# Optimization experiments

Hardware: AMD Instinct MI355X
Metric: run time of the kernel (lower is better)

Reference implementation:

```python
import jax
import jax.numpy as jnp
import numpy as np
from jax import lax

T, N, F_IN, H, E = 8, 10000, 128, 64, 160000


def setup_inputs() -> dict:
    key = jax.random.key(0)
    ks = jax.random.split(key, 8)
    s = 0.05
    return {
        "x": jax.random.normal(ks[0], (T, N, F_IN), jnp.float32),
        "edge_index": jax.random.randint(ks[1], (T, 2, E), 0, N, dtype=jnp.int64),
        "W_gcn": jax.random.normal(ks[2], (F_IN, H), jnp.float32) * s,
        "b_gcn": jnp.zeros((H,), jnp.float32),
        "W_ih": jax.random.normal(ks[3], (4 * H, H), jnp.float32) * s,
        "W_hh": jax.random.normal(ks[4], (4 * H, H), jnp.float32) * s,
        "b_ih": jnp.zeros((4 * H,), jnp.float32),
        "b_hh": jnp.zeros((4 * H,), jnp.float32),
    }


def _gcn_one(x, edge_index, W, b):
    # PyG GCNConv: transform then symmetric-normalized propagation with self-loops.
    h = x @ W  # [N, H]
    loop = jnp.arange(N, dtype=edge_index.dtype)
    src = jnp.concatenate([edge_index[0], loop])
    dst = jnp.concatenate([edge_index[1], loop])
    deg = jax.ops.segment_sum(jnp.ones_like(dst, dtype=h.dtype), dst, num_segments=N)
    dinv = lax.rsqrt(deg)  # deg >= 1 thanks to self-loops
    norm = dinv[src] * dinv[dst]  # [E+N]
    out = jax.ops.segment_sum(h[src] * norm[:, None], dst, num_segments=N)
    return out + b


def _lstm(xs, W_ih, W_hh, b_ih, b_hh):
    # batch_first LSTM: batch = T (graphs), sequence = N (nodes)
    xs_t = jnp.swapaxes(xs, 0, 1)  # [N, T, H]
    h0 = jnp.zeros((xs.shape[0], H), xs.dtype)
    c0 = jnp.zeros_like(h0)

    def step(carry, xt):
        h, c = carry
        gates = xt @ W_ih.T + b_ih + h @ W_hh.T + b_hh  # [T, 4H]
        i, f, g, o = jnp.split(gates, 4, axis=-1)  # torch gate order i,f,g,o
        i = jax.nn.sigmoid(i)
        f = jax.nn.sigmoid(f)
        g = jnp.tanh(g)
        o = jax.nn.sigmoid(o)
        c = f * c + i * g
        h = o * jnp.tanh(c)
        return (h, c), h

    _, hs = lax.scan(step, (h0, c0), xs_t)  # hs [N, T, H]
    return jnp.swapaxes(hs, 0, 1)  # [T, N, H]


def reference(x, edge_index, W_gcn, b_gcn, W_ih, W_hh, b_ih, b_hh):
    # per-graph GCNConv -> ReLU (dropout is identity in eval mode)
    gcn_out = jax.vmap(lambda xi, ei: _gcn_one(xi, ei, W_gcn, b_gcn))(x, edge_index)
    gcn_out = jax.nn.relu(gcn_out)  # [T, N, H]; squeeze(0) is a no-op for T>1
    return _lstm(gcn_out, W_ih, W_hh, b_ih, b_hh)
```

## Files before the change

kernel.cpp:

```cpp
#include <hip/hip_runtime.h>

#define Tn 8
#define Nn 10000
#define FIN 128
#define Hh 64
#define En 160000
#define NODES (Tn * Nn)
#define CAP 64

#define CHUNK 20
#define NCHT (Nn / CHUNK)
#define CHAINS (Tn * NCHT)
#define WARM 96
#define STEPS (WARM + CHUNK)

typedef _Float16 h8 __attribute__((ext_vector_type(8)));
typedef _Float16 h4 __attribute__((ext_vector_type(4)));
typedef float f4v __attribute__((ext_vector_type(4)));
typedef unsigned short u16x8 __attribute__((ext_vector_type(8)));

__device__ __forceinline__ float sigm(float x) {
    float e = __builtin_amdgcn_exp2f(-1.4426950408889634f * x);
    return __builtin_amdgcn_rcpf(1.0f + e);
}
__device__ __forceinline__ float tanh_(float x) {
    float e = __builtin_amdgcn_exp2f(2.8853900817779268f * x);
    return 1.0f - 2.0f * __builtin_amdgcn_rcpf(1.0f + e);
}

__device__ __forceinline__ int eget(const void* ei, int is32, size_t pos) {
    return is32 ? ((const int*)ei)[pos] : (int)((const long long*)ei)[pos];
}

__device__ __forceinline__ int detect32(const void* ei, int* s_aux) {
    unsigned aa = 0;
    for (int i = threadIdx.x; i < 4096; i += 256) aa |= ((const unsigned*)ei)[2 * i + 1];
    if (threadIdx.x == 0) *s_aux = 0;
    __syncthreads();
    if (aa) atomicOr(s_aux, 1);
    __syncthreads();
    return *s_aux;
}

__global__ void k_fill(const void* ei, int* cnt, unsigned short* elist) {
    __shared__ int s_aux;
    int is32 = detect32(ei, &s_aux);
    int t = blockIdx.x & 7;
    int e = (blockIdx.x >> 3) * 256 + threadIdx.x;
    int src = eget(ei, is32, (size_t)t * 2 * En + e);
    int dst = eget(ei, is32, (size_t)t * 2 * En + En + e);
    int node = t * Nn + dst;
    int pos = atomicAdd(&cnt[node], 1) & (CAP - 1);
    elist[(size_t)node * CAP + pos] = (unsigned short)src;
}

__global__ void k_gcn(const float* __restrict__ x, const float* __restrict__ Wg,
                      const int* __restrict__ cnt, float* __restrict__ dinv,
                      _Float16* __restrict__ hs) {
    __shared__ __align__(16) float smem[FIN * Hh + 16 * FIN];
    int tid = threadIdx.x;
    float* wl = smem;
    float* xs = smem + FIN * Hh;
    for (int i = tid; i < FIN * Hh / 4; i += 256)
        ((float4*)wl)[i] = ((const float4*)Wg)[i];
    int r0 = blockIdx.x * 16;
    const float4* x4 = (const float4*)(x + (size_t)r0 * FIN);
    ((float4*)xs)[tid] = x4[tid];
    ((float4*)xs)[tid + 256] = x4[tid + 256];
    __syncthreads();
    int cc = tid & 63, jg = tid >> 6;
    float acc[4] = {0.f, 0.f, 0.f, 0.f};
#pragma unroll 4
    for (int k = 0; k < FIN; k++) {
        float wv = wl[k * Hh + cc];
#pragma unroll
        for (int r = 0; r < 4; r++) acc[r] += xs[(jg * 4 + r) * FIN + k] * wv;
    }
#pragma unroll
    for (int r = 0; r < 4; r++) {
        int row = r0 + jg * 4 + r;
        float dv = rsqrtf((float)cnt[row] + 1.0f);
        if (cc == 0) dinv[row] = dv;
        hs[(size_t)row * Hh + cc] = (_Float16)(acc[r] * dv);
    }
}

__global__ void k_g(const int* __restrict__ cnt, const unsigned short* __restrict__ elist,
                    const _Float16* __restrict__ hs, const float* __restrict__ dinv,
                    const float* __restrict__ bg, _Float16* __restrict__ gbuf) {
    int tid = threadIdx.x;
    int jj = tid >> 4;
    int l16 = tid & 15;
    int grp = blockIdx.x * 16 + jj;
    int nedge = cnt[grp];
    const unsigned short* el = elist + (size_t)grp * CAP;
    const _Float16* ht = hs + (size_t)(grp / Nn) * Nn * Hh;
    float4 acc = {0.f, 0.f, 0.f, 0.f};
    for (int k = 0; k < nedge; k += 16) {
        u16x8 sa = *(const u16x8*)(el + k);
        u16x8 sb = *(const u16x8*)(el + k + 8);
        h4 v[16];
#pragma unroll
        for (int i = 0; i < 8; i++) v[i] = ((const h4*)(ht + (size_t)sa[i] * Hh))[l16];
#pragma unroll
        for (int i = 0; i < 8; i++) v[8 + i] = ((const h4*)(ht + (size_t)sb[i] * Hh))[l16];
#pragma unroll
        for (int i = 0; i < 16; i++) {
            float m = (k + i < nedge) ? 1.f : 0.f;
            acc.x += m * (float)v[i][0];
            acc.y += m * (float)v[i][1];
            acc.z += m * (float)v[i][2];
            acc.w += m * (float)v[i][3];
        }
    }
    float dd = dinv[grp];
    h4 hv = ((const h4*)(hs + (size_t)grp * Hh))[l16];
    float4 bgv = ((const float4*)bg)[l16];
    h4 gq;
    gq[0] = (_Float16)fmaxf((acc.x + (float)hv[0]) * dd + bgv.x, 0.f);
    gq[1] = (_Float16)fmaxf((acc.y + (float)hv[1]) * dd + bgv.y, 0.f);
    gq[2] = (_Float16)fmaxf((acc.z + (float)hv[2]) * dd + bgv.z, 0.f);
    gq[3] = (_Float16)fmaxf((acc.w + (float)hv[3]) * dd + bgv.w, 0.f);
    *(h4*)(gbuf + (size_t)grp * Hh + l16 * 4) = gq;
}

__global__ void __launch_bounds__(256, 1) k_lstm(const _Float16* __restrict__ gbuf,
                                                 const float* __restrict__ Wih,
                                                 const float* __restrict__ Whh,
                                                 const float* __restrict__ bih,
                                                 const float* __restrict__ bhh,
                                                 float* __restrict__ out) {
    __shared__ __align__(16) _Float16 hb[2][16][72];
    __shared__ __align__(16) _Float16 gb2[2][16][72];
    int tid = threadIdx.x;
    int w = tid >> 6;
    int lane = tid & 63;
    int l = lane & 15;
    int kg = lane >> 4;
    int col = w * 16 + l;

    h8 bh_[4][2], bg_[4][2];
    float bias[4];
#pragma unroll
    for (int q = 0; q < 4; q++) {
        int row = q * 64 + col;
        bias[q] = bih[row] + bhh[row];
#pragma unroll
        for (int half = 0; half < 2; half++) {
            const float* srch = Whh + (size_t)row * 64 + half * 32 + kg * 8;
            const float* srcg = Wih + (size_t)row * 64 + half * 32 + kg * 8;
            h8 th, tg;
#pragma unroll
            for (int j = 0; j < 8; j++) {
                th[j] = (_Float16)srch[j];
                tg[j] = (_Float16)srcg[j];
            }
            bh_[q][half] = th;
            bg_[q][half] = tg;
        }
    }

    float* ob[4];
    int nv[4], msk[4];
#pragma unroll
    for (int r = 0; r < 4; r++) {
        int g = blockIdx.x * 16 + 4 * kg + r;
        int tt = g / NCHT;
        int ch = g - tt * NCHT;
        nv[r] = ch * CHUNK - WARM;
        msk[r] = (ch == 0);
        ob[r] = out + (size_t)tt * Nn * 64 + col;
    }

    int sm = tid >> 4, sc = tid & 15;
    int gsid = blockIdx.x * 16 + sm;
    int stt = gsid / NCHT, sch = gsid - stt * NCHT;
    int nvs = sch * CHUNK - WARM;
    const _Float16* gp = gbuf + (size_t)stt * Nn * Hh + sc * 4;

    for (int i = tid; i < 2 * 16 * 72; i += 256) ((_Float16*)hb)[i] = (_Float16)0.f;
    {
        int n0 = nvs < 0 ? 0 : nvs;
        *(h4*)&gb2[0][sm][sc * 4] = *(const h4*)(gp + (size_t)n0 * Hh);
    }
    h4 pf[4];
#pragma unroll
    for (int d = 0; d < 4; d++) {
        int n = nvs + 1 + d;
        n = n < 0 ? 0 : (n > Nn - 1 ? Nn - 1 : n);
        pf[d] = *(const h4*)(gp + (size_t)n * Hh);
    }
    __syncthreads();

    float c0 = 0.f, c1 = 0.f, c2 = 0.f, c3 = 0.f;

#define MF(a, b, c) __builtin_amdgcn_mfma_f32_16x16x32_f16(a, b, c, 0, 0, 0)

#define GATES(r, cc, DO_STORE, s)                                \
    {                                                            \
        float iv = sigm(acc0[r]);                                \
        float fv = sigm(acc1[r]);                                \
        float gv = tanh_(acc2[r]);                               \
        float ov = sigm(acc3[r]);                                \
        cc = fv * cc + iv * gv;                                  \
        float hv = ov * tanh_(cc);                               \
        hb[((s) + 1) & 1][4 * kg + r][col] = (_Float16)hv;       \
        if (DO_STORE) ob[r][(size_t)(nv[r] + (s)) * 64] = hv;    \
    }

#define STEP(s, u, DO_STORE)                                                        \
    {                                                                               \
        h8 ah0 = *(const h8*)&hb[(s) & 1][l][kg * 8];                               \
        h8 ah1 = *(const h8*)&hb[(s) & 1][l][32 + kg * 8];                          \
        h8 ag0 = *(const h8*)&gb2[(s) & 1][l][kg * 8];                              \
        h8 ag1 = *(const h8*)&gb2[(s) & 1][l][32 + kg * 8];                         \
        f4v acc0 = {bias[0], bias[0], bias[0], bias[0]};                            \
        f4v acc1 = {bias[1], bias[1], bias[1], bias[1]};                            \
        f4v acc2 = {bias[2], bias[2], bias[2], bias[2]};                            \
        f4v acc3 = {bias[3], bias[3], bias[3], bias[3]};                            \
        acc0 = MF(ag0, bg_[0][0], acc0);                                            \
        acc1 = MF(ag0, bg_[1][0], acc1);                                            \
        acc2 = MF(ag0, bg_[2][0], acc2);                                            \
        acc3 = MF(ag0, bg_[3][0], acc3);                                            \
        acc0 = MF(ag1, bg_[0][1], acc0);                                            \
        acc1 = MF(ag1, bg_[1][1], acc1);                                            \
        acc2 = MF(ag1, bg_[2][1], acc2);                                            \
        acc3 = MF(ag1, bg_[3][1], acc3);                                            \
        acc0 = MF(ah0, bh_[0][0], acc0);                                            \
        acc1 = MF(ah0, bh_[1][0], acc1);                                            \
        acc2 = MF(ah0, bh_[2][0], acc2);                                            \
        acc3 = MF(ah0, bh_[3][0], acc3);                                            \
        acc0 = MF(ah1, bh_[0][1], acc0);                                            \
        acc1 = MF(ah1, bh_[1][1], acc1);                                            \
        acc2 = MF(ah1, bh_[2][1], acc2);                                            \
        acc3 = MF(ah1, bh_[3][1], acc3);                                            \
        *(h4*)&gb2[((s) + 1) & 1][sm][sc * 4] = pf[u];                              \
        {                                                                           \
            int np = nvs + (s) + 5;                                                 \
            np = np < 0 ? 0 : (np > Nn - 1 ? Nn - 1 : np);                          \
            pf[u] = *(const h4*)(gp + (size_t)np * Hh);                             \
        }                                                                           \
        GATES(0, c0, DO_STORE, s)                                                   \
        GATES(1, c1, DO_STORE, s)                                                   \
        GATES(2, c2, DO_STORE, s)                                                   \
        GATES(3, c3, DO_STORE, s)                                                   \
        asm volatile("s_waitcnt lgkmcnt(0)\n\ts_barrier" ::: "memory");             \
    }

    for (int s4 = 0; s4 < WARM; s4 += 4) {
        STEP(s4 + 0, 0, 0)
        STEP(s4 + 1, 1, 0)
        STEP(s4 + 2, 2, 0)
        STEP(s4 + 3, 3, 0)
    }
    if (msk[0]) { c0 = 0.f; hb[WARM & 1][4 * kg + 0][col] = (_Float16)0.f; }
    if (msk[1]) { c1 = 0.f; hb[WARM & 1][4 * kg + 1][col] = (_Float16)0.f; }
    if (msk[2]) { c2 = 0.f; hb[WARM & 1][4 * kg + 2][col] = (_Float16)0.f; }
    if (msk[3]) { c3 = 0.f; hb[WARM & 1][4 * kg + 3][col] = (_Float16)0.f; }
    asm volatile("s_waitcnt lgkmcnt(0)\n\ts_barrier" ::: "memory");
    for (int s4 = WARM; s4 < STEPS; s4 += 4) {
        STEP(s4 + 0, 0, 1)
        STEP(s4 + 1, 1, 1)
        STEP(s4 + 2, 2, 1)
        STEP(s4 + 3, 3, 1)
    }
#undef STEP
#undef GATES
#undef MF
}

extern "C" void kernel_launch(void* const* d_in, const int* in_sizes, int n_in,
                              void* d_out, int out_size, void* d_ws, size_t ws_size,
                              hipStream_t stream) {
    const float* x = (const float*)d_in[0];
    const void* ei = d_in[1];
    const float* Wg = (const float*)d_in[2];
    const float* bg = (const float*)d_in[3];
    const float* Wih = (const float*)d_in[4];
    const float* Whh = (const float*)d_in[5];
    const float* bih = (const float*)d_in[6];
    const float* bhh = (const float*)d_in[7];
    float* out = (float*)d_out;

    char* ws = (char*)d_ws;
    _Float16* gbuf = (_Float16*)(ws);
    _Float16* hs = (_Float16*)(ws + 10240000);
    float* dinv = (float*)(ws + 20480000);
    int* cnt = (int*)(ws + 20800000);
    unsigned short* elist = (unsigned short*)(ws + 21120000);

    hipMemsetAsync(cnt, 0, NODES * sizeof(int), stream);
    k_fill<<<Tn * En / 256, 256, 0, stream>>>(ei, cnt, elist);
    k_gcn<<<NODES / 16, 256, 0, stream>>>(x, Wg, cnt, dinv, hs);
    k_g<<<NODES / 16, 256, 0, stream>>>(cnt, elist, hs, dinv, bg, gbuf);
    k_lstm<<<CHAINS / 16, 256, 0, stream>>>(gbuf, Wih, Whh, bih, bhh, out);
}
```

Baseline: 280.9 us.

## Load LSTM input operands directly to registers and restructure GCN smem layout

The LSTM kernel no longer stages the GCN output through a shared-memory double buffer. Each lane loads its MFMA A-operand fragments straight from global memory into registers, prefetched two steps ahead. The input-projection MFMAs are issued before the h-dependent LDS reads, so they can overlap the previous step's hidden-state writes. The separate mask/barrier block at the warm-up boundary is replaced by an in-loop reset check. Separately, the GCN matmul transposes W into padded shared memory and uses float4 reads with explicit FMAs, which cuts the number of LDS instructions. The trade-off is a shorter prefetch distance, so global-load latency is less hidden in the serial recurrence.

```diff
diff --git a/kernel.cpp b/kernel.cpp
--- a/kernel.cpp
+++ b/kernel.cpp
@@ -57,24 +57,34 @@
 __global__ void k_gcn(const float* __restrict__ x, const float* __restrict__ Wg,
                       const int* __restrict__ cnt, float* __restrict__ dinv,
                       _Float16* __restrict__ hs) {
-    __shared__ __align__(16) float smem[FIN * Hh + 16 * FIN];
+    __shared__ __align__(16) float wl[64][132];
+    __shared__ __align__(16) float xs[16][132];
     int tid = threadIdx.x;
-    float* wl = smem;
-    float* xs = smem + FIN * Hh;
-    for (int i = tid; i < FIN * Hh / 4; i += 256)
-        ((float4*)wl)[i] = ((const float4*)Wg)[i];
+    for (int i = tid; i < FIN * Hh; i += 256) {
+        int k = i >> 6, c = i & 63;
+        wl[c][k] = Wg[i];
+    }
     int r0 = blockIdx.x * 16;
     const float4* x4 = (const float4*)(x + (size_t)r0 * FIN);
-    ((float4*)xs)[tid] = x4[tid];
-    ((float4*)xs)[tid + 256] = x4[tid + 256];
+    {
+        int i0 = tid, i1 = tid + 256;
+        *(float4*)&xs[i0 >> 5][(i0 & 31) * 4] = x4[i0];
+        *(float4*)&xs[i1 >> 5][(i1 & 31) * 4] = x4[i1];
+    }
     __syncthreads();
     int cc = tid & 63, jg = tid >> 6;
     float acc[4] = {0.f, 0.f, 0.f, 0.f};
-#pragma unroll 4
-    for (int k = 0; k < FIN; k++) {
-        float wv = wl[k * Hh + cc];
-#pragma unroll
-        for (int r = 0; r < 4; r++) acc[r] += xs[(jg * 4 + r) * FIN + k] * wv;
+#pragma unroll 8
+    for (int k = 0; k < FIN; k += 4) {
+        float4 wv = *(const float4*)&wl[cc][k];
+#pragma unroll
+        for (int r = 0; r < 4; r++) {
+            float4 xv = *(const float4*)&xs[jg * 4 + r][k];
+            acc[r] = __builtin_fmaf(wv.x, xv.x, acc[r]);
+            acc[r] = __builtin_fmaf(wv.y, xv.y, acc[r]);
+            acc[r] = __builtin_fmaf(wv.z, xv.z, acc[r]);
+            acc[r] = __builtin_fmaf(wv.w, xv.w, acc[r]);
+        }
     }
 #pragma unroll
     for (int r = 0; r < 4; r++) {
@@ -131,7 +141,6 @@
                                                  const float* __restrict__ bhh,
                                                  float* __restrict__ out) {
     __shared__ __align__(16) _Float16 hb[2][16][72];
-    __shared__ __align__(16) _Float16 gb2[2][16][72];
     int tid = threadIdx.x;
     int w = tid >> 6;
     int lane = tid & 63;
@@ -161,108 +170,98 @@
     }
 
     float* ob[4];
-    int nv[4], msk[4];
+    int nv[4], rst[4];
 #pragma unroll
     for (int r = 0; r < 4; r++) {
         int g = blockIdx.x * 16 + 4 * kg + r;
         int tt = g / NCHT;
         int ch = g - tt * NCHT;
         nv[r] = ch * CHUNK - WARM;
-        msk[r] = (ch == 0);
+        rst[r] = -nv[r];
         ob[r] = out + (size_t)tt * Nn * 64 + col;
     }
 
-    int sm = tid >> 4, sc = tid & 15;
-    int gsid = blockIdx.x * 16 + sm;
-    int stt = gsid / NCHT, sch = gsid - stt * NCHT;
-    int nvs = sch * CHUNK - WARM;
-    const _Float16* gp = gbuf + (size_t)stt * Nn * Hh + sc * 4;
+    int gid = blockIdx.x * 16 + l;
+    int gtt = gid / NCHT;
+    int gch = gid - gtt * NCHT;
+    int gnv = gch * CHUNK - WARM;
+    const _Float16* gb = gbuf + (size_t)gtt * Nn * Hh + kg * 8;
 
     for (int i = tid; i < 2 * 16 * 72; i += 256) ((_Float16*)hb)[i] = (_Float16)0.f;
+    __syncthreads();
+
+    h8 agA0, agA1, agB0, agB1;
     {
-        int n0 = nvs < 0 ? 0 : nvs;
-        *(h4*)&gb2[0][sm][sc * 4] = *(const h4*)(gp + (size_t)n0 * Hh);
-    }
-    h4 pf[4];
-#pragma unroll
-    for (int d = 0; d < 4; d++) {
-        int n = nvs + 1 + d;
-        n = n < 0 ? 0 : (n > Nn - 1 ? Nn - 1 : n);
-        pf[d] = *(const h4*)(gp + (size_t)n * Hh);
-    }
-    __syncthreads();
-
+        int n0 = gnv < 0 ? 0 : gnv;
+        agA0 = *(const h8*)(gb + (size_t)n0 * Hh);
+        agA1 = *(const h8*)(gb + (size_t)n0 * Hh + 32);
+        int n1 = gnv + 1;
+        n1 = n1 < 0 ? 0 : n1;
+        agB0 = *(const h8*)(gb + (size_t)n1 * Hh);
+        agB1 = *(const h8*)(gb + (size_t)n1 * Hh + 32);
+    }
     float c0 = 0.f, c1 = 0.f, c2 = 0.f, c3 = 0.f;
 
 #define MF(a, b, c) __builtin_amdgcn_mfma_f32_16x16x32_f16(a, b, c, 0, 0, 0)
 
-#define GATES(r, cc, DO_STORE, s)                                \
+#define GATES(r, cc, DO_STORE, s, P)                             \
     {                                                            \
-        float iv = sigm(acc0[r]);                                \
-        float fv = sigm(acc1[r]);                                \
-        float gv = tanh_(acc2[r]);                               \
-        float ov = sigm(acc3[r]);                                \
+        float iv = sigm(a0[r]);                                  \
+        float fv = sigm(a1[r]);                                  \
+        float gv = tanh_(a2[r]);                                 \
+        float ov = sigm(a3[r]);                                  \
         cc = fv * cc + iv * gv;                                  \
         float hv = ov * tanh_(cc);                               \
-        hb[((s) + 1) & 1][4 * kg + r][col] = (_Float16)hv;       \
+        if ((s) + 1 == rst[r]) { cc = 0.f; hv = 0.f; }           \
+        hb[(P) ^ 1][4 * kg + r][col] = (_Float16)hv;             \
         if (DO_STORE) ob[r][(size_t)(nv[r] + (s)) * 64] = hv;    \
     }
 
-#define STEP(s, u, DO_STORE)                                                        \
+#define STEP(s, P, G0, G1, DO_STORE)                                                \
     {                                                                               \
-        h8 ah0 = *(const h8*)&hb[(s) & 1][l][kg * 8];                               \
-        h8 ah1 = *(const h8*)&hb[(s) & 1][l][32 + kg * 8];                          \
-        h8 ag0 = *(const h8*)&gb2[(s) & 1][l][kg * 8];                              \
-        h8 ag1 = *(const h8*)&gb2[(s) & 1][l][32 + kg * 8];                         \
-        f4v acc0 = {bias[0], bias[0], bias[0], bias[0]};                            \
-        f4v acc1 = {bias[1], bias[1], bias[1], bias[1]};                            \
-        f4v acc2 = {bias[2], bias[2], bias[2], bias[2]};                            \
-        f4v acc3 = {bias[3], bias[3], bias[3], bias[3]};                            \
-        acc0 = MF(ag0, bg_[0][0], acc0);                                            \
-        acc1 = MF(ag0, bg_[1][0], acc1);                                            \
-        acc2 = MF(ag0, bg_[2][0], acc2);                                            \
-        acc3 = MF(ag0, bg_[3][0], acc3);                                            \
-        acc0 = MF(ag1, bg_[0][1], acc0);                                            \
-        acc1 = MF(ag1, bg_[1][1], acc1);                                            \
-        acc2 = MF(ag1, bg_[2][1], acc2);                                            \
-        acc3 = MF(ag1, bg_[3][1], acc3);                                            \
-        acc0 = MF(ah0, bh_[0][0], acc0);                                            \
-        acc1 = MF(ah0, bh_[1][0], acc1);                                            \
-        acc2 = MF(ah0, bh_[2][0], acc2);                                            \
-        acc3 = MF(ah0, bh_[3][0], acc3);                                            \
-        acc0 = MF(ah1, bh_[0][1], acc0);                                            \
-        acc1 = MF(ah1, bh_[1][1], acc1);                                            \
-        acc2 = MF(ah1, bh_[2][1], acc2);                                            \
-        acc3 = MF(ah1, bh_[3][1], acc3);                                            \
-        *(h4*)&gb2[((s) + 1) & 1][sm][sc * 4] = pf[u];                              \
+        f4v a0 = {bias[0], bias[0], bias[0], bias[0]};                              \
+        f4v a1 = {bias[1], bias[1], bias[1], bias[1]};                              \
+        f4v a2 = {bias[2], bias[2], bias[2], bias[2]};                              \
+        f4v a3 = {bias[3], bias[3], bias[3], bias[3]};                              \
+        a0 = MF(G0, bg_[0][0], a0);                                                 \
+        a1 = MF(G0, bg_[1][0], a1);                                                 \
+        a2 = MF(G0, bg_[2][0], a2);                                                 \
+        a3 = MF(G0, bg_[3][0], a3);                                                 \
+        a0 = MF(G1, bg_[0][1], a0);                                                 \
+        a1 = MF(G1, bg_[1][1], a1);                                                 \
+        a2 = MF(G1, bg_[2][1], a2);                                                 \
+        a3 = MF(G1, bg_[3][1], a3);                                                 \
         {                                                                           \
-            int np = nvs + (s) + 5;                                                 \
+            int np = gnv + (s) + 2;                                                 \
             np = np < 0 ? 0 : (np > Nn - 1 ? Nn - 1 : np);                          \
-            pf[u] = *(const h4*)(gp + (size_t)np * Hh);                             \
+            const _Float16* gq = gb + (size_t)np * Hh;                              \
+            G0 = *(const h8*)gq;                                                    \
+            G1 = *(const h8*)(gq + 32);                                             \
         }                                                                           \
-        GATES(0, c0, DO_STORE, s)                                                   \
-        GATES(1, c1, DO_STORE, s)                                                   \
-        GATES(2, c2, DO_STORE, s)                                                   \
-        GATES(3, c3, DO_STORE, s)                                                   \
+        h8 ah0 = *(const h8*)&hb[P][l][kg * 8];                                     \
+        h8 ah1 = *(const h8*)&hb[P][l][32 + kg * 8];                                \
+        a0 = MF(ah0, bh_[0][0], a0);                                                \
+        a1 = MF(ah0, bh_[1][0], a1);                                                \
+        a2 = MF(ah0, bh_[2][0], a2);                                                \
+        a3 = MF(ah0, bh_[3][0], a3);                                                \
+        a0 = MF(ah1, bh_[0][1], a0);                                                \
+        a1 = MF(ah1, bh_[1][1], a1);                                                \
+        a2 = MF(ah1, bh_[2][1], a2);                                                \
+        a3 = MF(ah1, bh_[3][1], a3);                                                \
+        GATES(0, c0, DO_STORE, s, P)                                                \
+        GATES(1, c1, DO_STORE, s, P)                                                \
+        GATES(2, c2, DO_STORE, s, P)                                                \
+        GATES(3, c3, DO_STORE, s, P)                                                \
         asm volatile("s_waitcnt lgkmcnt(0)\n\ts_barrier" ::: "memory");             \
     }
 
-    for (int s4 = 0; s4 < WARM; s4 += 4) {
-        STEP(s4 + 0, 0, 0)
-        STEP(s4 + 1, 1, 0)
-        STEP(s4 + 2, 2, 0)
-        STEP(s4 + 3, 3, 0)
-    }
-    if (msk[0]) { c0 = 0.f; hb[WARM & 1][4 * kg + 0][col] = (_Float16)0.f; }
-    if (msk[1]) { c1 = 0.f; hb[WARM & 1][4 * kg + 1][col] = (_Float16)0.f; }
-    if (msk[2]) { c2 = 0.f; hb[WARM & 1][4 * kg + 2][col] = (_Float16)0.f; }
-    if (msk[3]) { c3 = 0.f; hb[WARM & 1][4 * kg + 3][col] = (_Float16)0.f; }
-    asm volatile("s_waitcnt lgkmcnt(0)\n\ts_barrier" ::: "memory");
-    for (int s4 = WARM; s4 < STEPS; s4 += 4) {
-        STEP(s4 + 0, 0, 1)
-        STEP(s4 + 1, 1, 1)
-        STEP(s4 + 2, 2, 1)
-        STEP(s4 + 3, 3, 1)
+    for (int s2 = 0; s2 < WARM; s2 += 2) {
+        STEP(s2 + 0, 0, agA0, agA1, 0)
+        STEP(s2 + 1, 1, agB0, agB1, 0)
+    }
+    for (int s2 = WARM; s2 < STEPS; s2 += 2) {
+        STEP(s2 + 0, 0, agA0, agA1, 1)
+        STEP(s2 + 1, 1, agB0, agB1, 1)
     }
 #undef STEP
 #undef GATES
```

Result: no change. 286.2 us (+1.9%).
